# Kernel optimization log

Measured on AMD Instinct MI355X. Metric: run time of the kernel, lower is better.

The kernel has to match this reference:

```python
import jax, jax.numpy as jnp
import numpy as np

B, V, E, L, D = 4, 64, 1024, 1024, 256  # batch, vertices, edges/graph, seq_len, d_model
DEG = E // V


def setup_inputs() -> dict:
    key = jax.random.key(0)
    k0, k1, k2, k3, k4, k5 = jax.random.split(key, 6)
    # fixed 16-regular graph, edges sorted by (src, dst) so that nonzero()
    # extraction order of the dense adjacency equals a gather at (src, dst)
    src = np.repeat(np.arange(V), DEG)
    dst = (src + 1 + np.tile(np.arange(DEG), V)) % V
    order = np.lexsort((dst, src))
    src, dst = src[order], dst[order]
    edge_index = jnp.asarray(np.stack([np.tile(src, B), np.tile(dst, B)]), dtype=jnp.int32)
    hidden_states = jax.random.normal(k0, (B * V, L, D), dtype=jnp.float32)
    edge_weight = jax.random.uniform(k1, (B * E,), dtype=jnp.float32, minval=0.1, maxval=1.0)
    s = 0.02
    Wq = jax.random.normal(k2, (D, D), dtype=jnp.float32) * s
    bq = jax.random.normal(k3, (D,), dtype=jnp.float32) * s
    Wk = jax.random.normal(k4, (D, D), dtype=jnp.float32) * s
    bk = jax.random.normal(k5, (D,), dtype=jnp.float32) * s
    attn_skip = jnp.float32(0.5)
    return {"hidden_states": hidden_states, "edge_index": edge_index, "edge_weight": edge_weight,
            "Wq": Wq, "bq": bq, "Wk": Wk, "bk": bk, "attn_skip": attn_skip}


def reference(hidden_states, edge_index, edge_weight, Wq, bq, Wk, bk, attn_skip):
    # broadcast static edge list / weights across time, as the torch repeat does
    ei = jnp.broadcast_to(edge_index[:, :, None], (2, B * E, L))
    ew = jnp.broadcast_to(edge_weight[:, None], (B * E, L))
    hs = hidden_states.reshape(B, V, L, D)
    Q = hs @ Wq.T + bq  # nn.Linear: x W^T + b
    K = hs @ Wk.T + bk
    att = jnp.einsum('bvld,bwld->bvwl', Q, K) / jnp.sqrt(jnp.float32(D))
    bidx = jnp.repeat(jnp.arange(B), E)
    src, dst = edge_index[0], edge_index[1]
    # to_dense_adj: scatter-add edge weights -> (B, V, V, L)
    adj = jnp.zeros((B, V, V, L), att.dtype).at[bidx, src, dst, :].add(ew)
    mask = jnp.where(adj > 0, 0.0, -jnp.inf)
    att = jax.nn.softmax(att + mask, axis=2)  # softmax over destination vertices w
    adj_new = attn_skip * adj + (1.0 - attn_skip) * att
    # dense_to_sparse: nonzeros in (graph=b*L+l, row, col) row-major order.
    # Edges are sorted by (src,dst), so this is a gather; torch flat order is (b, l, e):
    g = adj_new[bidx, src, dst, :]  # (B*E, L) ordered (b, e, l)
    flat = g.reshape(B, E, L).transpose(0, 2, 1).reshape(-1)  # order (b, l, e)
    # replicate the original .view(B, E, L).transpose(1, 2).reshape(B*E, L)
    ew_out = flat.reshape(B, E, L).transpose(0, 2, 1).reshape(B * E, L)
    return ei, ew_out
```

## Files before the change

kernel.cpp:

```cpp
#include <hip/hip_runtime.h>
#include <cstdint>
#include <cstddef>

constexpr int Bv = 4;
constexpr int Ev = 1024;
constexpr int Lv = 1024;
constexpr int BE = Bv * Ev;
constexpr size_t EI_PLANE = (size_t)BE * Lv;

constexpr int STRB = 264;

typedef __bf16 bf16x8 __attribute__((ext_vector_type(8)));
typedef __bf16 bf16x4 __attribute__((ext_vector_type(4)));
typedef __bf16 bf16x2 __attribute__((ext_vector_type(2)));
typedef float  f32x4  __attribute__((ext_vector_type(4)));

static __device__ __forceinline__ unsigned int pack_bf2(float lo, float hi) {
    union { bf16x2 h; unsigned int u; } c;
    c.h[0] = (__bf16)lo; c.h[1] = (__bf16)hi;
    return c.u;
}

__global__ __launch_bounds__(256) void precompute_kernel(
    const float* __restrict__ Wq, const float* __restrict__ Wk,
    const float* __restrict__ bq, __bf16* __restrict__ Mb, float* __restrict__ rv)
{
    const int blk = blockIdx.x;
    const int tid = threadIdx.x;
    if (blk < 256) {
        __shared__ float qs[256 * 17];
        __shared__ float ks[256 * 17];
        const int i16 = (blk >> 4) * 16;
        const int j16 = (blk & 15) * 16;
        const int c  = tid & 15;
        const int r0 = tid >> 4;
        #pragma unroll
        for (int it = 0; it < 16; ++it) {
            const int r = it * 16 + r0;
            qs[r * 17 + c] = Wq[r * 256 + i16 + c];
            ks[r * 17 + c] = Wk[r * 256 + j16 + c];
        }
        __syncthreads();
        const int dd = tid >> 4;
        const int tt = tid & 15;
        float a0 = 0.f, a1 = 0.f, a2 = 0.f, a3 = 0.f;
        for (int r = 0; r < 256; r += 4) {
            a0 = fmaf(qs[(r + 0) * 17 + dd], ks[(r + 0) * 17 + tt], a0);
            a1 = fmaf(qs[(r + 1) * 17 + dd], ks[(r + 1) * 17 + tt], a1);
            a2 = fmaf(qs[(r + 2) * 17 + dd], ks[(r + 2) * 17 + tt], a2);
            a3 = fmaf(qs[(r + 3) * 17 + dd], ks[(r + 3) * 17 + tt], a3);
        }
        const float m = ((a0 + a1) + (a2 + a3)) * 0.0625f;
        const int d = i16 + dd, t = j16 + tt;
        const int f    = (d >> 5) * 16 + (t >> 4);
        const int lane = ((d >> 3) & 3) * 16 + (t & 15);
        const int jj   = d & 7;
        Mb[((size_t)f * 64 + lane) * 8 + jj] = (__bf16)m;
    } else {
        __shared__ float bqs[256];
        bqs[tid] = bq[tid];
        __syncthreads();
        float a0 = 0.f, a1 = 0.f;
        for (int i = 0; i < 256; i += 2) {
            a0 = fmaf(bqs[i + 0], Wk[(i + 0) * 256 + tid], a0);
            a1 = fmaf(bqs[i + 1], Wk[(i + 1) * 256 + tid], a1);
        }
        rv[tid] = (a0 + a1) * 0.0625f;
    }
}

template <bool USE_WS>
__global__ __launch_bounds__(256, 4) void edge_main(
    const float* __restrict__ hs, const int* __restrict__ eidx,
    const float* __restrict__ ew, const float* __restrict__ skipp,
    const __bf16* __restrict__ Mb, const float* __restrict__ rv,
    float* __restrict__ probs_or_out)
{
    __shared__ __bf16 hs_s[64 * STRB];
    float* S0 = (float*)hs_s;

    const int bl = blockIdx.x;
    const int b  = bl >> 10;
    const int l  = bl & 1023;
    const int tid  = threadIdx.x;
    const int w    = tid >> 6;
    const int lane = tid & 63;
    const int l15  = lane & 15;
    const int quad = lane >> 4;
    const int nt1  = (w + 1) & 3;

    const int e0  = tid * 4;
    const int be0 = b * Ev + e0;
    int soff[4];
    #pragma unroll
    for (int j = 0; j < 4; ++j) {
        const int src = eidx[be0 + j];
        const int dst = eidx[BE + be0 + j];
        const int slot = ((dst >> 4) - (src >> 4)) & 3;
        soff[j] = src * 36 + slot * 16 + (dst & 15);
    }

    {
        const float* base = hs + ((size_t)b * 64 * 1024 + (size_t)l) * 256;
        const int half = lane >> 5;
        const int c8   = (lane & 31) * 8;
        #pragma unroll
        for (int k = 0; k < 8; ++k) {
            const int v = k * 8 + w * 2 + half;
            const float* p = base + (size_t)v * (1024 * 256) + c8;
            float4 va = *(const float4*)p;
            float4 vb = *(const float4*)(p + 4);
            bf16x8 h;
            h[0] = (__bf16)va.x; h[1] = (__bf16)va.y;
            h[2] = (__bf16)va.z; h[3] = (__bf16)va.w;
            h[4] = (__bf16)vb.x; h[5] = (__bf16)vb.y;
            h[6] = (__bf16)vb.z; h[7] = (__bf16)vb.w;
            *(bf16x8*)(&hs_s[v * STRB + c8]) = h;
        }
    }
    __syncthreads();

    bf16x8 hfrK[8];
    #pragma unroll
    for (int kt = 0; kt < 8; ++kt)
        hfrK[kt] = *(const bf16x8*)(&hs_s[(w * 16 + l15) * STRB + kt * 32 + quad * 8]);

    f32x4 s_acc0, s_acc1;
    s_acc0[0] = 0.f; s_acc0[1] = 0.f; s_acc0[2] = 0.f; s_acc0[3] = 0.f;
    s_acc1 = s_acc0;

    #pragma unroll 1
    for (int p = 0; p < 8; ++p) {
        f32x4 acc0 = *(const f32x4*)(rv + (2 * p + 0) * 16 + quad * 4);
        f32x4 acc1 = *(const f32x4*)(rv + (2 * p + 1) * 16 + quad * 4);
        #pragma unroll
        for (int kh = 0; kh < 2; ++kh) {
            bf16x8 m0[4], m1[4];
            #pragma unroll
            for (int k2 = 0; k2 < 4; ++k2) {
                const int kt = kh * 4 + k2;
                m0[k2] = *(const bf16x8*)(Mb +
                    ((size_t)((kt * 16 + 2 * p + 0) * 64 + lane)) * 8);
                m1[k2] = *(const bf16x8*)(Mb +
                    ((size_t)((kt * 16 + 2 * p + 1) * 64 + lane)) * 8);
            }
            #pragma unroll
            for (int k2 = 0; k2 < 4; ++k2) {
                const int kt = kh * 4 + k2;
                acc0 = __builtin_amdgcn_mfma_f32_16x16x32_bf16(
                    m0[k2], hfrK[kt], acc0, 0, 0, 0);
                acc1 = __builtin_amdgcn_mfma_f32_16x16x32_bf16(
                    m1[k2], hfrK[kt], acc1, 0, 0, 0);
            }
        }
        unsigned int Ar = pack_bf2(acc0[0], acc0[1]);
        unsigned int Br = pack_bf2(acc0[2], acc0[3]);
        unsigned int Cr = pack_bf2(acc1[0], acc1[1]);
        unsigned int Dr = pack_bf2(acc1[2], acc1[3]);
        asm("v_permlane32_swap_b32 %0, %1" : "+v"(Ar), "+v"(Cr));
        asm("v_permlane16_swap_b32 %0, %1" : "+v"(Ar), "+v"(Cr));
        asm("v_permlane32_swap_b32 %0, %1" : "+v"(Br), "+v"(Dr));
        asm("v_permlane16_swap_b32 %0, %1" : "+v"(Br), "+v"(Dr));
        union { uint4 u; bf16x8 h; } fr;
        fr.u = make_uint4(Ar, Br, Cr, Dr);

        const bf16x8 brow0 = *(const bf16x8*)(
            &hs_s[(w * 16 + l15) * STRB + p * 32 + quad * 8]);
        const bf16x8 brow1 = *(const bf16x8*)(
            &hs_s[(nt1 * 16 + l15) * STRB + p * 32 + quad * 8]);
        s_acc0 = __builtin_amdgcn_mfma_f32_16x16x32_bf16(fr.h, brow0, s_acc0, 0, 0, 0);
        s_acc1 = __builtin_amdgcn_mfma_f32_16x16x32_bf16(fr.h, brow1, s_acc1, 0, 0, 0);
    }
    __syncthreads();

    #pragma unroll
    for (int r = 0; r < 4; ++r) {
        S0[(w * 16 + quad * 4 + r) * 36 +  0 + l15] = s_acc0[r];
        S0[(w * 16 + quad * 4 + r) * 36 + 16 + l15] = s_acc1[r];
    }
    __syncthreads();

    float lg[4];
    #pragma unroll
    for (int j = 0; j < 4; ++j)
        lg[j] = S0[soff[j]];

    float mx = fmaxf(fmaxf(lg[0], lg[1]), fmaxf(lg[2], lg[3]));
    mx = fmaxf(mx, __shfl_xor(mx, 1));
    mx = fmaxf(mx, __shfl_xor(mx, 2));
    float ex[4], sm = 0.f;
    #pragma unroll
    for (int j = 0; j < 4; ++j) { ex[j] = __expf(lg[j] - mx); sm += ex[j]; }
    sm += __shfl_xor(sm, 1);
    sm += __shfl_xor(sm, 2);
    const float inv = 1.0f / sm;

    if (USE_WS) {
        float4 o = make_float4(ex[0] * inv, ex[1] * inv, ex[2] * inv, ex[3] * inv);
        *(float4*)(probs_or_out + (size_t)bl * 1024 + e0) = o;
    } else {
        const float skip = skipp[0];
        const float om = 1.0f - skip;
        #pragma unroll
        for (int j = 0; j < 4; ++j) {
            float g = fmaf(skip, ew[be0 + j], om * (ex[j] * inv));
            probs_or_out[(size_t)(be0 + j) * Lv + l] = g;
        }
    }
}

__global__ __launch_bounds__(256) void output_kernel(
    const float* __restrict__ probs, const int* __restrict__ eidx,
    const float* __restrict__ ew, const float* __restrict__ skipp,
    float* __restrict__ out)
{
    __shared__ float tile[64 * 68];
    const int lt = blockIdx.x;
    const int et = blockIdx.y;
    const int b  = blockIdx.z;
    const int t  = threadIdx.x;
    const int tr = t >> 4;
    const int tc = t & 15;

    #pragma unroll
    for (int q = 0; q < 4; ++q) {
        const int lloc = q * 16 + tr;
        float4 v = *(const float4*)(probs +
            ((size_t)(b * 1024 + lt * 64 + lloc)) * 1024 + et * 64 + tc * 4);
        *(float4*)(&tile[lloc * 68 + tc * 4]) = v;
    }
    __syncthreads();

    const float skip = skipp[0];
    const float om = 1.0f - skip;
    float* out_ei0 = out;
    float* out_ei1 = out + EI_PLANE;
    float* out_ew  = out + 2 * EI_PLANE;

    #pragma unroll
    for (int q = 0; q < 4; ++q) {
        const int eloc = q * 16 + tr;
        const int be = b * Ev + et * 64 + eloc;
        const float w  = ew[be];
        const float sv = (float)eidx[be];
        const float dv = (float)eidx[BE + be];
        const int lloc0 = tc * 4;
        float4 o;
        o.x = fmaf(skip, w, om * tile[(lloc0 + 0) * 68 + eloc]);
        o.y = fmaf(skip, w, om * tile[(lloc0 + 1) * 68 + eloc]);
        o.z = fmaf(skip, w, om * tile[(lloc0 + 2) * 68 + eloc]);
        o.w = fmaf(skip, w, om * tile[(lloc0 + 3) * 68 + eloc]);
        const size_t off = (size_t)be * Lv + lt * 64 + lloc0;
        *(float4*)(out_ew  + off) = o;
        *(float4*)(out_ei0 + off) = make_float4(sv, sv, sv, sv);
        *(float4*)(out_ei1 + off) = make_float4(dv, dv, dv, dv);
    }
}

__global__ __launch_bounds__(256) void ei_kernel(
    const int* __restrict__ eidx, float* __restrict__ out)
{
    const int blk = blockIdx.x;
    const int c = blk >> 12;
    const int j = blk & 4095;
    const float v = (float)eidx[c * BE + j];
    float4 o = make_float4(v, v, v, v);
    *(float4*)(out + (size_t)blk * 1024 + threadIdx.x * 4) = o;
}

extern "C" void kernel_launch(void* const* d_in, const int* in_sizes, int n_in,
                              void* d_out, int out_size, void* d_ws, size_t ws_size,
                              hipStream_t stream)
{
    const float* hs   = (const float*)d_in[0];
    const int*   eidx = (const int*)d_in[1];
    const float* ew   = (const float*)d_in[2];
    const float* Wq   = (const float*)d_in[3];
    const float* bq   = (const float*)d_in[4];
    const float* Wk   = (const float*)d_in[5];
    const float* skip = (const float*)d_in[7];

    char* wsb = (char*)d_ws;
    __bf16* Mb   = (__bf16*)wsb;
    float*  rv   = (float*)(wsb + 131072);
    float*  probs = (float*)(wsb + 132096);
    const size_t need = 132096 + (size_t)Bv * Lv * Ev * sizeof(float);

    precompute_kernel<<<dim3(257), dim3(256), 0, stream>>>(Wq, Wk, bq, Mb, rv);

    if (ws_size >= need) {
        edge_main<true><<<dim3(Bv * Lv), dim3(256), 0, stream>>>(
            hs, eidx, ew, skip, Mb, rv, probs);
        output_kernel<<<dim3(16, 16, 4), dim3(256), 0, stream>>>(
            probs, eidx, ew, skip, (float*)d_out);
    } else {
        float* out_ew = (float*)d_out + 2 * EI_PLANE;
        edge_main<false><<<dim3(Bv * Lv), dim3(256), 0, stream>>>(
            hs, eidx, ew, skip, Mb, rv, out_ew);
        ei_kernel<<<dim3(2 * BE), dim3(256), 0, stream>>>(eidx, (float*)d_out);
    }
}
```

Before: 451.7 us.

## Load hidden-state fragments directly from global memory, dropping LDS staging

Each wave now converts its own 16 hidden-state rows, and its partner wave's rows, straight from global memory into bf16 MFMA fragments. This replaces staging all 64 rows through shared memory, and it drops the block-wide barriers, since each wave only reads logits it wrote itself. Shared memory shrinks to a small logit tile, so the launch bound rises to 5 blocks per CU, and the projection loop is fully unrolled. The cost is that partner rows are fetched from global twice, once by each wave that needs them, which relies on L2 to absorb the extra traffic and adds register pressure.

```diff
diff --git a/kernel.cpp b/kernel.cpp
--- a/kernel.cpp
+++ b/kernel.cpp
@@ -8,10 +8,9 @@
 constexpr int BE = Bv * Ev;
 constexpr size_t EI_PLANE = (size_t)BE * Lv;
 
-constexpr int STRB = 264;
+constexpr int SROW = 33;
 
 typedef __bf16 bf16x8 __attribute__((ext_vector_type(8)));
-typedef __bf16 bf16x4 __attribute__((ext_vector_type(4)));
 typedef __bf16 bf16x2 __attribute__((ext_vector_type(2)));
 typedef float  f32x4  __attribute__((ext_vector_type(4)));
 
@@ -19,6 +18,17 @@
     union { bf16x2 h; unsigned int u; } c;
     c.h[0] = (__bf16)lo; c.h[1] = (__bf16)hi;
     return c.u;
+}
+
+static __device__ __forceinline__ bf16x8 load_frag8(const float* p) {
+    float4 a = *(const float4*)p;
+    float4 b = *(const float4*)(p + 4);
+    union { uint4 u; bf16x8 h; } t;
+    t.u.x = pack_bf2(a.x, a.y);
+    t.u.y = pack_bf2(a.z, a.w);
+    t.u.z = pack_bf2(b.x, b.y);
+    t.u.w = pack_bf2(b.z, b.w);
+    return t.h;
 }
 
 __global__ __launch_bounds__(256) void precompute_kernel(
@@ -70,14 +80,13 @@
 }
 
 template <bool USE_WS>
-__global__ __launch_bounds__(256, 4) void edge_main(
+__global__ __launch_bounds__(256, 5) void edge_main(
     const float* __restrict__ hs, const int* __restrict__ eidx,
     const float* __restrict__ ew, const float* __restrict__ skipp,
     const __bf16* __restrict__ Mb, const float* __restrict__ rv,
     float* __restrict__ probs_or_out)
 {
-    __shared__ __bf16 hs_s[64 * STRB];
-    float* S0 = (float*)hs_s;
+    __shared__ float S0[64 * SROW];
 
     const int bl = blockIdx.x;
     const int b  = bl >> 10;
@@ -97,62 +106,45 @@
         const int src = eidx[be0 + j];
         const int dst = eidx[BE + be0 + j];
         const int slot = ((dst >> 4) - (src >> 4)) & 3;
-        soff[j] = src * 36 + slot * 16 + (dst & 15);
-    }
-
-    {
-        const float* base = hs + ((size_t)b * 64 * 1024 + (size_t)l) * 256;
-        const int half = lane >> 5;
-        const int c8   = (lane & 31) * 8;
-        #pragma unroll
-        for (int k = 0; k < 8; ++k) {
-            const int v = k * 8 + w * 2 + half;
-            const float* p = base + (size_t)v * (1024 * 256) + c8;
-            float4 va = *(const float4*)p;
-            float4 vb = *(const float4*)(p + 4);
-            bf16x8 h;
-            h[0] = (__bf16)va.x; h[1] = (__bf16)va.y;
-            h[2] = (__bf16)va.z; h[3] = (__bf16)va.w;
-            h[4] = (__bf16)vb.x; h[5] = (__bf16)vb.y;
-            h[6] = (__bf16)vb.z; h[7] = (__bf16)vb.w;
-            *(bf16x8*)(&hs_s[v * STRB + c8]) = h;
-        }
-    }
-    __syncthreads();
+        soff[j] = src * SROW + slot * 16 + (dst & 15);
+    }
+
+    const float* rb_own = hs +
+        ((size_t)(b * 64 + w * 16 + l15) * 1024 + (size_t)l) * 256;
+    const float* rb_par = hs +
+        ((size_t)(b * 64 + nt1 * 16 + l15) * 1024 + (size_t)l) * 256;
 
     bf16x8 hfrK[8];
     #pragma unroll
     for (int kt = 0; kt < 8; ++kt)
-        hfrK[kt] = *(const bf16x8*)(&hs_s[(w * 16 + l15) * STRB + kt * 32 + quad * 8]);
+        hfrK[kt] = load_frag8(rb_own + kt * 32 + quad * 8);
 
     f32x4 s_acc0, s_acc1;
     s_acc0[0] = 0.f; s_acc0[1] = 0.f; s_acc0[2] = 0.f; s_acc0[3] = 0.f;
     s_acc1 = s_acc0;
 
-    #pragma unroll 1
+    #pragma unroll
     for (int p = 0; p < 8; ++p) {
         f32x4 acc0 = *(const f32x4*)(rv + (2 * p + 0) * 16 + quad * 4);
         f32x4 acc1 = *(const f32x4*)(rv + (2 * p + 1) * 16 + quad * 4);
         #pragma unroll
-        for (int kh = 0; kh < 2; ++kh) {
-            bf16x8 m0[4], m1[4];
-            #pragma unroll
-            for (int k2 = 0; k2 < 4; ++k2) {
-                const int kt = kh * 4 + k2;
-                m0[k2] = *(const bf16x8*)(Mb +
-                    ((size_t)((kt * 16 + 2 * p + 0) * 64 + lane)) * 8);
-                m1[k2] = *(const bf16x8*)(Mb +
-                    ((size_t)((kt * 16 + 2 * p + 1) * 64 + lane)) * 8);
-            }
-            #pragma unroll
-            for (int k2 = 0; k2 < 4; ++k2) {
-                const int kt = kh * 4 + k2;
-                acc0 = __builtin_amdgcn_mfma_f32_16x16x32_bf16(
-                    m0[k2], hfrK[kt], acc0, 0, 0, 0);
-                acc1 = __builtin_amdgcn_mfma_f32_16x16x32_bf16(
-                    m1[k2], hfrK[kt], acc1, 0, 0, 0);
-            }
-        }
+        for (int kh = 0; kh < 4; ++kh) {
+            const int kta = kh * 2, ktb = kh * 2 + 1;
+            const bf16x8 m0a = *(const bf16x8*)(Mb +
+                ((size_t)((kta * 16 + 2 * p + 0) * 64 + lane)) * 8);
+            const bf16x8 m1a = *(const bf16x8*)(Mb +
+                ((size_t)((kta * 16 + 2 * p + 1) * 64 + lane)) * 8);
+            const bf16x8 m0b = *(const bf16x8*)(Mb +
+                ((size_t)((ktb * 16 + 2 * p + 0) * 64 + lane)) * 8);
+            const bf16x8 m1b = *(const bf16x8*)(Mb +
+                ((size_t)((ktb * 16 + 2 * p + 1) * 64 + lane)) * 8);
+            acc0 = __builtin_amdgcn_mfma_f32_16x16x32_bf16(m0a, hfrK[kta], acc0, 0, 0, 0);
+            acc1 = __builtin_amdgcn_mfma_f32_16x16x32_bf16(m1a, hfrK[kta], acc1, 0, 0, 0);
+            acc0 = __builtin_amdgcn_mfma_f32_16x16x32_bf16(m0b, hfrK[ktb], acc0, 0, 0, 0);
+            acc1 = __builtin_amdgcn_mfma_f32_16x16x32_bf16(m1b, hfrK[ktb], acc1, 0, 0, 0);
+        }
+        const bf16x8 brow1 = load_frag8(rb_par + p * 32 + quad * 8);
+
         unsigned int Ar = pack_bf2(acc0[0], acc0[1]);
         unsigned int Br = pack_bf2(acc0[2], acc0[3]);
         unsigned int Cr = pack_bf2(acc1[0], acc1[1]);
@@ -164,21 +156,15 @@
         union { uint4 u; bf16x8 h; } fr;
         fr.u = make_uint4(Ar, Br, Cr, Dr);
 
-        const bf16x8 brow0 = *(const bf16x8*)(
-            &hs_s[(w * 16 + l15) * STRB + p * 32 + quad * 8]);
-        const bf16x8 brow1 = *(const bf16x8*)(
-            &hs_s[(nt1 * 16 + l15) * STRB + p * 32 + quad * 8]);
-        s_acc0 = __builtin_amdgcn_mfma_f32_16x16x32_bf16(fr.h, brow0, s_acc0, 0, 0, 0);
-        s_acc1 = __builtin_amdgcn_mfma_f32_16x16x32_bf16(fr.h, brow1, s_acc1, 0, 0, 0);
-    }
-    __syncthreads();
+        s_acc0 = __builtin_amdgcn_mfma_f32_16x16x32_bf16(fr.h, hfrK[p], s_acc0, 0, 0, 0);
+        s_acc1 = __builtin_amdgcn_mfma_f32_16x16x32_bf16(fr.h, brow1,   s_acc1, 0, 0, 0);
+    }
 
     #pragma unroll
     for (int r = 0; r < 4; ++r) {
-        S0[(w * 16 + quad * 4 + r) * 36 +  0 + l15] = s_acc0[r];
-        S0[(w * 16 + quad * 4 + r) * 36 + 16 + l15] = s_acc1[r];
-    }
-    __syncthreads();
+        S0[(w * 16 + quad * 4 + r) * SROW +  0 + l15] = s_acc0[r];
+        S0[(w * 16 + quad * 4 + r) * SROW + 16 + l15] = s_acc1[r];
+    }
 
     float lg[4];
     #pragma unroll
```

Result: slower. 525.2 us (+16.3%).
